# Kernel optimization log

Hardware: AMD Instinct MI355X
Metric: run time of the kernel (lower is better)

Reference implementation:

```python
import jax, jax.numpy as jnp
import numpy as np

N = 96
M = 96
# visual field constants
L_V_EX, S_V_EX, L_V_IN, S_V_IN = 1.6, 3.5, 1.23, 6.3
FV, TAU_V, UPS_V, P_V, K_V = 1.0, 3.0, 3.0, 0.3, 7.0
# auditory field constants
L_A_EX, S_A_EX, L_A_IN, S_A_IN = 1.0, 5.3, 0.8, 11.8
FA, TAU_A, UPS_A, P_A, K_A = 1.0, 3.0, 3.0, 0.3, 3.0
# multisensory field constants
L_M_EX, S_M_EX, L_M_IN, S_M_IN = 3.8, 3.5, 3.3, 6.2
TAU_M, UPS_M, P_M = 3.0, 3.0, 0.3


def _torus_sqdist():
    # squared toroidal distance components: dx2[i,h], dy2[j,k]
    ii = jnp.arange(N, dtype=jnp.float32)
    jj = jnp.arange(M, dtype=jnp.float32)
    dx = jnp.abs(ii[:, None] - ii[None, :])
    dx = jnp.minimum(dx, N - dx)
    dy = jnp.abs(jj[:, None] - jj[None, :])
    dy = jnp.minimum(dy, M - dy)
    # aux[i,j,h,k] = dx[i,h]^2 + dy[j,k]^2
    return dx[:, None, :, None] ** 2 + dy[None, :, None, :] ** 2


def _dog(aux, l_ex, s_ex, l_in, s_in):
    # Faithful to source: exp(-aux/2 * sigma**2) == exp(-0.5*aux*sigma^2)
    return l_ex * jnp.exp(-0.5 * aux * (s_ex ** 2)) - l_in * jnp.exp(-0.5 * aux * (s_in ** 2))


def setup_inputs() -> dict:
    key = jax.random.key(0)
    ks = jax.random.split(key, 7)
    return {
        "video": jax.random.normal(ks[0], (32, 1024), dtype=jnp.float32),
        "audio": jax.random.normal(ks[1], (32, 2048), dtype=jnp.float32),
        "rf_v": jax.random.normal(ks[2], (N, M, 1024), dtype=jnp.float32) * (1.0 / np.sqrt(1024.0)),
        "rf_a": jax.random.normal(ks[3], (N, M, 2048), dtype=jnp.float32) * (1.0 / np.sqrt(2048.0)),
        "na_v": jax.random.normal(ks[4], (N, M), dtype=jnp.float32),
        "na_a": jax.random.normal(ks[5], (N, M), dtype=jnp.float32),
        "na_m": jax.random.normal(ks[6], (N, M), dtype=jnp.float32),
    }


def reference(video, audio, rf_v, rf_a, na_v, na_a, na_m):
    aux = _torus_sqdist()  # (N, M, N, M)
    syn_v = _dog(aux, L_V_EX, S_V_EX, L_V_IN, S_V_IN)
    syn_a = _dog(aux, L_A_EX, S_A_EX, L_A_IN, S_A_IN)
    syn_m = _dog(aux, L_M_EX, S_M_EX, L_M_IN, S_M_IN)

    # external inputs: sum over feature dim -> (B, N, M)
    ext_v = jnp.einsum('bv,ijv->bij', video, rf_v)
    ext_a = jnp.einsum('ba,ija->bij', audio, rf_a)

    # all-pairs neighbor inputs: neighbor[i,j] = sum_{h,k} act[h,k] * syn[i,j,h,k]
    nb_v = jnp.einsum('ijhk,hk->ij', syn_v, na_v)
    nb_a = jnp.einsum('ijhk,hk->ij', syn_a, na_a)

    coll_v = FV * na_m
    coll_a = FA * na_m

    na_v_new = na_v * (TAU_V - 1.0) / TAU_V + (1.0 / TAU_V) * jax.nn.sigmoid(
        (ext_v + nb_v - UPS_V + coll_v) * P_V)  # (B, N, M)
    na_a_new = na_a * (TAU_A - 1.0) / TAU_A + (1.0 / TAU_A) * jax.nn.sigmoid(
        (ext_a + nb_a - UPS_A + coll_a) * P_A)  # (B, N, M)

    nb_m = jnp.einsum('ijhk,hk->ij', syn_m, na_m)
    na_m_new = na_m * (TAU_M - 1.0) / TAU_M + (1.0 / TAU_M) * jax.nn.sigmoid(
        (K_V * na_v_new + K_A * na_a_new + nb_m - UPS_M) * P_M)  # (B, N, M)
    return na_m_new
```

## Files before the change

kernel.cpp:

```cpp
#include <hip/hip_runtime.h>
#include <math.h>

#define NN   96
#define NPOS (96*96)
#define BB   32
#define KV   1024
#define KA   2048

#define EXTV_OFF  0
#define EXTA0_OFF (BB*NPOS)
#define EXTA1_OFF (2*BB*NPOS)
#define CPT_OFF   (3*BB*NPOS)
#define AFV_OFF   (CPT_OFF + 6*NPOS)
#define AFV_SLOTS ((KV/32)*2*64)
#define AFA_OFF   (AFV_OFF + AFV_SLOTS*4)
#define AFA_SLOTS ((KA/32)*2*64)

typedef __bf16 bf16x8 __attribute__((ext_vector_type(8)));
typedef __bf16 bf16x4 __attribute__((ext_vector_type(4)));
typedef float  f32x4  __attribute__((ext_vector_type(4)));

__global__ __launch_bounds__(256) void nbT_kernel(
    const float* __restrict__ na_v, const float* __restrict__ na_a,
    const float* __restrict__ na_m, const float* __restrict__ video,
    const float* __restrict__ audio, float* __restrict__ ws)
{
    __shared__ float G[96][100];
    __shared__ float act_s[96][100];
    __shared__ float T1t[24][100];

    if (blockIdx.x >= 24) {
        const int e = (blockIdx.x - 24) * 256 + threadIdx.x;
        const float* src; bf16x8* dst; int K, el;
        if (e < AFV_SLOTS) { src = video; K = KV; dst = (bf16x8*)(ws + AFV_OFF); el = e; }
        else               { src = audio; K = KA; dst = (bf16x8*)(ws + AFA_OFF); el = e - AFV_SLOTS; }
        const int l  = el & 63;
        const int hb = (el >> 6) & 1;
        const int sg = el >> 7;
        const int b  = hb * 16 + (l & 15);
        const int k0 = sg * 32 + ((l >> 4) << 3);
        const float4 f0 = *(const float4*)&src[(size_t)b * K + k0];
        const float4 f1 = *(const float4*)&src[(size_t)b * K + k0 + 4];
        bf16x8 v;
        v[0] = (__bf16)f0.x; v[1] = (__bf16)f0.y; v[2] = (__bf16)f0.z; v[3] = (__bf16)f0.w;
        v[4] = (__bf16)f1.x; v[5] = (__bf16)f1.y; v[6] = (__bf16)f1.z; v[7] = (__bf16)f1.w;
        dst[el] = v;
        return;
    }

    const int c  = blockIdx.x >> 2;
    const int js = (blockIdx.x & 3) * 24;
    float l, s;
    if      (c == 0) { l =  1.60f; s = 3.5f;  }
    else if (c == 1) { l = -1.23f; s = 6.3f;  }
    else if (c == 2) { l =  1.00f; s = 5.3f;  }
    else if (c == 3) { l = -0.80f; s = 11.8f; }
    else if (c == 4) { l =  3.80f; s = 3.5f;  }
    else             { l = -3.30f; s = 6.2f;  }
    const float s2 = s * s;
    const int f = c >> 1;
    const float* act = (f == 0) ? na_v : (f == 1) ? na_a : na_m;
    const int tid = threadIdx.x;
    float* cpt = ws + CPT_OFF;

    for (int idx = tid; idx < 9216; idx += 256) {
        int j = idx / 96, k = idx - j * 96;
        int d = abs(j - k); d = min(d, 96 - d);
        G[j][k]     = __expf(-0.5f * (float)(d * d) * s2);
        act_s[j][k] = act[idx];
    }
    __syncthreads();

    const int hg3 = (tid >> 3) * 3;
    const int jl3 = (tid & 7) * 3;

    float t1[3][3] = {};
    for (int k0 = 0; k0 < 96; k0 += 4) {
        float4 av[3], gv[3];
        #pragma unroll
        for (int r = 0; r < 3; r++) {
            av[r] = *(const float4*)&act_s[hg3 + r][k0];
            gv[r] = *(const float4*)&G[js + jl3 + r][k0];
        }
        #pragma unroll
        for (int hh = 0; hh < 3; hh++)
            #pragma unroll
            for (int jj = 0; jj < 3; jj++)
                t1[hh][jj] += av[hh].x * gv[jj].x + av[hh].y * gv[jj].y
                            + av[hh].z * gv[jj].z + av[hh].w * gv[jj].w;
    }
    #pragma unroll
    for (int hh = 0; hh < 3; hh++)
        #pragma unroll
        for (int jj = 0; jj < 3; jj++)
            T1t[jl3 + jj][hg3 + hh] = t1[hh][jj];
    __syncthreads();

    float o[3][3] = {};
    for (int h0 = 0; h0 < 96; h0 += 4) {
        float4 gv[3], tv[3];
        #pragma unroll
        for (int r = 0; r < 3; r++) {
            gv[r] = *(const float4*)&G[hg3 + r][h0];
            tv[r] = *(const float4*)&T1t[jl3 + r][h0];
        }
        #pragma unroll
        for (int ii = 0; ii < 3; ii++)
            #pragma unroll
            for (int jj = 0; jj < 3; jj++)
                o[ii][jj] += gv[ii].x * tv[jj].x + gv[ii].y * tv[jj].y
                           + gv[ii].z * tv[jj].z + gv[ii].w * tv[jj].w;
    }
    #pragma unroll
    for (int ii = 0; ii < 3; ii++)
        #pragma unroll
        for (int jj = 0; jj < 3; jj++)
            cpt[c * NPOS + (hg3 + ii) * 96 + (js + jl3 + jj)] = l * o[ii][jj];
}

#define LDS_ROW 2064
#define RED_OFF (16*LDS_ROW)
__global__ __launch_bounds__(512, 4) void ext_mfma(
    const float* __restrict__ rf_v, const float* __restrict__ rf_a,
    float* __restrict__ ws)
{
    __shared__ char lds[16 * LDS_ROW + 6144];
    const int tid = threadIdx.x;
    const int bid = blockIdx.x;

    const float* rf; const bf16x8* af; float* ext; int K, kb, pt;
    if (bid < 1152) {
        const int c = bid / 576; pt = bid - c * 576;
        rf = rf_a; K = KA; kb = c << 10;
        af  = (const bf16x8*)(ws + AFA_OFF);
        ext = ws + EXTA0_OFF + c * (BB * NPOS);
    } else {
        pt = bid - 1152; rf = rf_v; K = KV; kb = 0;
        af  = (const bf16x8*)(ws + AFV_OFF);
        ext = ws + EXTV_OFF;
    }

    {
        const int r0 = tid >> 8;
        const int c4 = (tid & 255) * 4;
        float4 fa[8];
        #pragma unroll
        for (int u = 0; u < 8; ++u)
            fa[u] = *(const float4*)(rf + (size_t)(pt * 16 + r0 + 2 * u) * K + kb + c4);
        #pragma unroll
        for (int u = 0; u < 8; ++u) {
            bf16x4 v;
            v[0] = (__bf16)fa[u].x; v[1] = (__bf16)fa[u].y;
            v[2] = (__bf16)fa[u].z; v[3] = (__bf16)fa[u].w;
            *(bf16x4*)(lds + (r0 + 2 * u) * LDS_ROW + c4 * 2) = v;
        }
    }
    __syncthreads();

    const int l  = tid & 63, w = tid >> 6;
    const int bh = w & 1, kq = w >> 1;
    const bf16x8* ap = af + ((kb >> 5) + kq * 8) * 128 + (bh << 6) + l;
    const char*   bp = lds + (l & 15) * LDS_ROW + kq * 512 + ((l >> 4) << 4);

    bf16x8 a0 = ap[0 * 128], a1 = ap[1 * 128], a2 = ap[2 * 128], a3 = ap[3 * 128];
    bf16x8 a4 = ap[4 * 128], a5 = ap[5 * 128], a6 = ap[6 * 128], a7 = ap[7 * 128];
    bf16x8 b0 = *(const bf16x8*)(bp + 0 * 64), b1 = *(const bf16x8*)(bp + 1 * 64);
    bf16x8 b2 = *(const bf16x8*)(bp + 2 * 64), b3 = *(const bf16x8*)(bp + 3 * 64);
    bf16x8 b4 = *(const bf16x8*)(bp + 4 * 64), b5 = *(const bf16x8*)(bp + 5 * 64);
    bf16x8 b6 = *(const bf16x8*)(bp + 6 * 64), b7 = *(const bf16x8*)(bp + 7 * 64);

    f32x4 acc = {0.f, 0.f, 0.f, 0.f};
    acc = __builtin_amdgcn_mfma_f32_16x16x32_bf16(a0, b0, acc, 0, 0, 0);
    acc = __builtin_amdgcn_mfma_f32_16x16x32_bf16(a1, b1, acc, 0, 0, 0);
    acc = __builtin_amdgcn_mfma_f32_16x16x32_bf16(a2, b2, acc, 0, 0, 0);
    acc = __builtin_amdgcn_mfma_f32_16x16x32_bf16(a3, b3, acc, 0, 0, 0);
    acc = __builtin_amdgcn_mfma_f32_16x16x32_bf16(a4, b4, acc, 0, 0, 0);
    acc = __builtin_amdgcn_mfma_f32_16x16x32_bf16(a5, b5, acc, 0, 0, 0);
    acc = __builtin_amdgcn_mfma_f32_16x16x32_bf16(a6, b6, acc, 0, 0, 0);
    acc = __builtin_amdgcn_mfma_f32_16x16x32_bf16(a7, b7, acc, 0, 0, 0);

    if (kq) *(f32x4*)(lds + RED_OFF + (((kq - 1) << 1) + bh) * 1024 + l * 16) = acc;
    __syncthreads();
    if (!kq) {
        #pragma unroll
        for (int q = 0; q < 3; ++q)
            acc += *(const f32x4*)(lds + RED_OFF + ((q << 1) + bh) * 1024 + l * 16);
        const int pcol = pt * 16 + (l & 15);
        const int br0  = (bh << 4) + ((l >> 4) << 2);
        #pragma unroll
        for (int r = 0; r < 4; ++r)
            ext[(size_t)(br0 + r) * NPOS + pcol] = acc[r];
    }
}

__global__ __launch_bounds__(256) void combine_kernel(
    const float* __restrict__ na_v, const float* __restrict__ na_a,
    const float* __restrict__ na_m, const float* __restrict__ ws,
    float* __restrict__ out)
{
    const int npq = NPOS >> 2;
    const int t = blockIdx.x * 256 + threadIdx.x;
    if (t >= BB * npq) return;
    const int b  = t / npq;
    const int p0 = (t - b * npq) << 2;

    float4 ev  = *(const float4*)&ws[EXTV_OFF  + (size_t)b * NPOS + p0];
    float4 ea0 = *(const float4*)&ws[EXTA0_OFF + (size_t)b * NPOS + p0];
    float4 ea1 = *(const float4*)&ws[EXTA1_OFF + (size_t)b * NPOS + p0];
    float4 ea = {ea0.x + ea1.x, ea0.y + ea1.y, ea0.z + ea1.z, ea0.w + ea1.w};
    const float* cpt = ws + CPT_OFF;
    float4 q0 = *(const float4*)&cpt[0 * NPOS + p0];
    float4 q1 = *(const float4*)&cpt[1 * NPOS + p0];
    float4 q2 = *(const float4*)&cpt[2 * NPOS + p0];
    float4 q3 = *(const float4*)&cpt[3 * NPOS + p0];
    float4 q4 = *(const float4*)&cpt[4 * NPOS + p0];
    float4 q5 = *(const float4*)&cpt[5 * NPOS + p0];
    float4 nv = *(const float4*)&na_v[p0];
    float4 na = *(const float4*)&na_a[p0];
    float4 nm = *(const float4*)&na_m[p0];

    float evs[4] = {ev.x, ev.y, ev.z, ev.w};
    float eas[4] = {ea.x, ea.y, ea.z, ea.w};
    float nbv[4] = {q0.x + q1.x, q0.y + q1.y, q0.z + q1.z, q0.w + q1.w};
    float nba[4] = {q2.x + q3.x, q2.y + q3.y, q2.z + q3.z, q2.w + q3.w};
    float nbm[4] = {q4.x + q5.x, q4.y + q5.y, q4.z + q5.z, q4.w + q5.w};
    float nvs[4] = {nv.x, nv.y, nv.z, nv.w};
    float nas[4] = {na.x, na.y, na.z, na.w};
    float nms[4] = {nm.x, nm.y, nm.z, nm.w};

    float4 o;
    float* os = (float*)&o;
    #pragma unroll
    for (int u = 0; u < 4; u++) {
        const float xv = (evs[u] + nbv[u] - 3.0f + nms[u]) * 0.3f;
        const float nav_new = nvs[u] * (2.f / 3.f) + (1.f / 3.f) / (1.f + __expf(-xv));
        const float xa = (eas[u] + nba[u] - 3.0f + nms[u]) * 0.3f;
        const float naa_new = nas[u] * (2.f / 3.f) + (1.f / 3.f) / (1.f + __expf(-xa));
        const float xm = (7.0f * nav_new + 3.0f * naa_new + nbm[u] - 3.0f) * 0.3f;
        os[u] = nms[u] * (2.f / 3.f) + (1.f / 3.f) / (1.f + __expf(-xm));
    }
    *(float4*)&out[(size_t)b * NPOS + p0] = o;
}

extern "C" void kernel_launch(void* const* d_in, const int* in_sizes, int n_in,
                              void* d_out, int out_size, void* d_ws, size_t ws_size,
                              hipStream_t stream) {
    const float* video = (const float*)d_in[0];
    const float* audio = (const float*)d_in[1];
    const float* rf_v  = (const float*)d_in[2];
    const float* rf_a  = (const float*)d_in[3];
    const float* na_v  = (const float*)d_in[4];
    const float* na_a  = (const float*)d_in[5];
    const float* na_m  = (const float*)d_in[6];
    float* ws  = (float*)d_ws;
    float* out = (float*)d_out;

    nbT_kernel<<<72, 256, 0, stream>>>(na_v, na_a, na_m, video, audio, ws);
    ext_mfma<<<1728, 512, 0, stream>>>(rf_v, rf_a, ws);
    combine_kernel<<<(BB * NPOS / 4 + 255) / 256, 256, 0, stream>>>(
        na_v, na_a, na_m, ws, out);
}
```

Measured before the change: 38.08 us.

## Merge ext GEMM blocks per position tile with double-buffered LDS pipeline

The ext_mfma kernel now launches one block per 16-position tile, replacing the earlier three blocks per tile (two audio K halves plus video). Each block walks six K-chunks of 512 through a double-buffered LDS stage, overlapping the global loads of the next chunk with the MFMA work on the current one. Because the audio result is reduced within a single block, the separate EXTA1 partial buffer is no longer needed and combine_kernel reads one audio value instead of two. The cost is fewer blocks (576), so less parallelism to hide memory latency on a large GPU, plus more barriers per block.

Result: slower. 44.71 us (+17.4%).

```diff
diff --git a/kernel.cpp b/kernel.cpp
--- a/kernel.cpp
+++ b/kernel.cpp
@@ -8,7 +8,7 @@
 #define KA   2048
 
 #define EXTV_OFF  0
-#define EXTA0_OFF (BB*NPOS)
+#define EXTA_OFF  (BB*NPOS)
 #define EXTA1_OFF (2*BB*NPOS)
 #define CPT_OFF   (3*BB*NPOS)
 #define AFV_OFF   (CPT_OFF + 6*NPOS)
@@ -118,79 +118,130 @@
             cpt[c * NPOS + (hg3 + ii) * 96 + (js + jl3 + jj)] = l * o[ii][jj];
 }
 
-#define LDS_ROW 2064
-#define RED_OFF (16*LDS_ROW)
+#define LROW 1040
+#define BUFSZ (16*LROW)
+#define REDOFF (2*BUFSZ)
 __global__ __launch_bounds__(512, 4) void ext_mfma(
     const float* __restrict__ rf_v, const float* __restrict__ rf_a,
     float* __restrict__ ws)
 {
-    __shared__ char lds[16 * LDS_ROW + 6144];
+    __shared__ char lds[2 * BUFSZ + 6144];
     const int tid = threadIdx.x;
-    const int bid = blockIdx.x;
-
-    const float* rf; const bf16x8* af; float* ext; int K, kb, pt;
-    if (bid < 1152) {
-        const int c = bid / 576; pt = bid - c * 576;
-        rf = rf_a; K = KA; kb = c << 10;
-        af  = (const bf16x8*)(ws + AFA_OFF);
-        ext = ws + EXTA0_OFF + c * (BB * NPOS);
-    } else {
-        pt = bid - 1152; rf = rf_v; K = KV; kb = 0;
-        af  = (const bf16x8*)(ws + AFV_OFF);
-        ext = ws + EXTV_OFF;
-    }
-
-    {
-        const int r0 = tid >> 8;
-        const int c4 = (tid & 255) * 4;
-        float4 fa[8];
-        #pragma unroll
-        for (int u = 0; u < 8; ++u)
-            fa[u] = *(const float4*)(rf + (size_t)(pt * 16 + r0 + 2 * u) * K + kb + c4);
-        #pragma unroll
-        for (int u = 0; u < 8; ++u) {
-            bf16x4 v;
-            v[0] = (__bf16)fa[u].x; v[1] = (__bf16)fa[u].y;
-            v[2] = (__bf16)fa[u].z; v[3] = (__bf16)fa[u].w;
-            *(bf16x4*)(lds + (r0 + 2 * u) * LDS_ROW + c4 * 2) = v;
-        }
-    }
-    __syncthreads();
-
+    const int pt  = blockIdx.x;
+    const int p0  = pt * 16;
+
+    const int r    = tid >> 7;
+    const int c128 = tid & 127;
     const int l  = tid & 63, w = tid >> 6;
     const int bh = w & 1, kq = w >> 1;
-    const bf16x8* ap = af + ((kb >> 5) + kq * 8) * 128 + (bh << 6) + l;
-    const char*   bp = lds + (l & 15) * LDS_ROW + kq * 512 + ((l >> 4) << 4);
-
-    bf16x8 a0 = ap[0 * 128], a1 = ap[1 * 128], a2 = ap[2 * 128], a3 = ap[3 * 128];
-    bf16x8 a4 = ap[4 * 128], a5 = ap[5 * 128], a6 = ap[6 * 128], a7 = ap[7 * 128];
-    bf16x8 b0 = *(const bf16x8*)(bp + 0 * 64), b1 = *(const bf16x8*)(bp + 1 * 64);
-    bf16x8 b2 = *(const bf16x8*)(bp + 2 * 64), b3 = *(const bf16x8*)(bp + 3 * 64);
-    bf16x8 b4 = *(const bf16x8*)(bp + 4 * 64), b5 = *(const bf16x8*)(bp + 5 * 64);
-    bf16x8 b6 = *(const bf16x8*)(bp + 6 * 64), b7 = *(const bf16x8*)(bp + 7 * 64);
-
-    f32x4 acc = {0.f, 0.f, 0.f, 0.f};
-    acc = __builtin_amdgcn_mfma_f32_16x16x32_bf16(a0, b0, acc, 0, 0, 0);
-    acc = __builtin_amdgcn_mfma_f32_16x16x32_bf16(a1, b1, acc, 0, 0, 0);
-    acc = __builtin_amdgcn_mfma_f32_16x16x32_bf16(a2, b2, acc, 0, 0, 0);
-    acc = __builtin_amdgcn_mfma_f32_16x16x32_bf16(a3, b3, acc, 0, 0, 0);
-    acc = __builtin_amdgcn_mfma_f32_16x16x32_bf16(a4, b4, acc, 0, 0, 0);
-    acc = __builtin_amdgcn_mfma_f32_16x16x32_bf16(a5, b5, acc, 0, 0, 0);
-    acc = __builtin_amdgcn_mfma_f32_16x16x32_bf16(a6, b6, acc, 0, 0, 0);
-    acc = __builtin_amdgcn_mfma_f32_16x16x32_bf16(a7, b7, acc, 0, 0, 0);
-
-    if (kq) *(f32x4*)(lds + RED_OFF + (((kq - 1) << 1) + bh) * 1024 + l * 16) = acc;
-    __syncthreads();
-    if (!kq) {
-        #pragma unroll
-        for (int q = 0; q < 3; ++q)
-            acc += *(const f32x4*)(lds + RED_OFF + ((q << 1) + bh) * 1024 + l * 16);
-        const int pcol = pt * 16 + (l & 15);
-        const int br0  = (bh << 4) + ((l >> 4) << 2);
-        #pragma unroll
-        for (int r = 0; r < 4; ++r)
-            ext[(size_t)(br0 + r) * NPOS + pcol] = acc[r];
-    }
+    const int rb_off = (l & 15) * LROW + kq * 256 + ((l >> 4) << 4);
+
+    const float*  sb[6];
+    const bf16x8* ab[6];
+    {
+        const float* ra = rf_a + (size_t)(p0 + r) * KA + c128 * 4;
+        const float* rv = rf_v + (size_t)(p0 + r) * KV + c128 * 4;
+        sb[0] = ra;        sb[1] = ra + 512;
+        sb[2] = ra + 1024; sb[3] = ra + 1536;
+        sb[4] = rv;        sb[5] = rv + 512;
+        const bf16x8* aa = (const bf16x8*)(ws + AFA_OFF) + kq * 4 * 128 + (bh << 6) + l;
+        const bf16x8* av = (const bf16x8*)(ws + AFV_OFF) + kq * 4 * 128 + (bh << 6) + l;
+        ab[0] = aa;        ab[1] = aa + 16 * 128;
+        ab[2] = aa + 32 * 128; ab[3] = aa + 48 * 128;
+        ab[4] = av;        ab[5] = av + 16 * 128;
+    }
+
+    float4 fa0, fa1, fa2, fa3;
+    bf16x8 xA0, xA1, xA2, xA3, xB0, xB1, xB2, xB3;
+    f32x4 accA = {0.f, 0.f, 0.f, 0.f};
+    f32x4 accV = {0.f, 0.f, 0.f, 0.f};
+
+#define STAGE(S, KK) do {                                         \
+        fa0 = *(const float4*)(sb[S]);                            \
+        fa1 = *(const float4*)(sb[S] + 4  * (size_t)(KK));        \
+        fa2 = *(const float4*)(sb[S] + 8  * (size_t)(KK));        \
+        fa3 = *(const float4*)(sb[S] + 12 * (size_t)(KK));        \
+    } while (0)
+
+#define CVT4(F) ({ bf16x4 v_;                                     \
+        v_[0] = (__bf16)(F).x; v_[1] = (__bf16)(F).y;             \
+        v_[2] = (__bf16)(F).z; v_[3] = (__bf16)(F).w; v_; })
+
+#define WWRITE(S) do {                                            \
+        char* bw = lds + ((S) & 1) * BUFSZ + c128 * 8;            \
+        *(bf16x4*)(bw + (r +  0) * LROW) = CVT4(fa0);             \
+        *(bf16x4*)(bw + (r +  4) * LROW) = CVT4(fa1);             \
+        *(bf16x4*)(bw + (r +  8) * LROW) = CVT4(fa2);             \
+        *(bf16x4*)(bw + (r + 12) * LROW) = CVT4(fa3);             \
+    } while (0)
+
+#define AFLD(S, A0, A1, A2, A3) do {                              \
+        const bf16x8* ap_ = ab[S];                                \
+        A0 = ap_[0]; A1 = ap_[128]; A2 = ap_[256]; A3 = ap_[384]; \
+    } while (0)
+
+#define COMP(S, ACC, A0, A1, A2, A3) do {                                      \
+        const char* br = lds + ((S) & 1) * BUFSZ + rb_off;                     \
+        bf16x8 b0 = *(const bf16x8*)(br);                                      \
+        bf16x8 b1 = *(const bf16x8*)(br + 64);                                 \
+        bf16x8 b2 = *(const bf16x8*)(br + 128);                                \
+        bf16x8 b3 = *(const bf16x8*)(br + 192);                                \
+        ACC = __builtin_amdgcn_mfma_f32_16x16x32_bf16(A0, b0, ACC, 0, 0, 0);   \
+        ACC = __builtin_amdgcn_mfma_f32_16x16x32_bf16(A1, b1, ACC, 0, 0, 0);   \
+        ACC = __builtin_amdgcn_mfma_f32_16x16x32_bf16(A2, b2, ACC, 0, 0, 0);   \
+        ACC = __builtin_amdgcn_mfma_f32_16x16x32_bf16(A3, b3, ACC, 0, 0, 0);   \
+    } while (0)
+
+#define BARL do {                                                 \
+        asm volatile("s_waitcnt lgkmcnt(0)" ::: "memory");        \
+        __builtin_amdgcn_sched_barrier(0);                        \
+        __builtin_amdgcn_s_barrier();                             \
+        __builtin_amdgcn_sched_barrier(0);                        \
+    } while (0)
+
+#define REDUCE(ACC, EXTP) do {                                                 \
+        if (kq) *(f32x4*)(lds + REDOFF + (((kq - 1) << 1) + bh) * 1024         \
+                          + l * 16) = ACC;                                     \
+        BARL;                                                                  \
+        if (!kq) {                                                             \
+            ACC += *(const f32x4*)(lds + REDOFF + (0 * 2 + bh) * 1024 + l*16); \
+            ACC += *(const f32x4*)(lds + REDOFF + (1 * 2 + bh) * 1024 + l*16); \
+            ACC += *(const f32x4*)(lds + REDOFF + (2 * 2 + bh) * 1024 + l*16); \
+            const int pcol = p0 + (l & 15);                                    \
+            const int br0  = (bh << 4) + ((l >> 4) << 2);                      \
+            float* ep = (EXTP);                                                \
+            ep[(size_t)(br0 + 0) * NPOS + pcol] = ACC[0];                      \
+            ep[(size_t)(br0 + 1) * NPOS + pcol] = ACC[1];                      \
+            ep[(size_t)(br0 + 2) * NPOS + pcol] = ACC[2];                      \
+            ep[(size_t)(br0 + 3) * NPOS + pcol] = ACC[3];                      \
+        }                                                                      \
+    } while (0)
+
+    STAGE(0, KA); AFLD(0, xA0, xA1, xA2, xA3);
+    WWRITE(0);
+    STAGE(1, KA);
+    BARL;
+    COMP(0, accA, xA0, xA1, xA2, xA3); AFLD(1, xB0, xB1, xB2, xB3);
+    WWRITE(1); STAGE(2, KA); BARL;
+    COMP(1, accA, xB0, xB1, xB2, xB3); AFLD(2, xA0, xA1, xA2, xA3);
+    WWRITE(2); STAGE(3, KA); BARL;
+    COMP(2, accA, xA0, xA1, xA2, xA3); AFLD(3, xB0, xB1, xB2, xB3);
+    WWRITE(3); STAGE(4, KV); BARL;
+    COMP(3, accA, xB0, xB1, xB2, xB3); AFLD(4, xA0, xA1, xA2, xA3);
+    REDUCE(accA, ws + EXTA_OFF);
+    WWRITE(4); STAGE(5, KV); BARL;
+    COMP(4, accV, xA0, xA1, xA2, xA3); AFLD(5, xB0, xB1, xB2, xB3);
+    WWRITE(5); BARL;
+    COMP(5, accV, xB0, xB1, xB2, xB3);
+    REDUCE(accV, ws + EXTV_OFF);
+
+#undef STAGE
+#undef CVT4
+#undef WWRITE
+#undef AFLD
+#undef COMP
+#undef BARL
+#undef REDUCE
 }
 
 __global__ __launch_bounds__(256) void combine_kernel(
@@ -204,10 +255,8 @@
     const int b  = t / npq;
     const int p0 = (t - b * npq) << 2;
 
-    float4 ev  = *(const float4*)&ws[EXTV_OFF  + (size_t)b * NPOS + p0];
-    float4 ea0 = *(const float4*)&ws[EXTA0_OFF + (size_t)b * NPOS + p0];
-    float4 ea1 = *(const float4*)&ws[EXTA1_OFF + (size_t)b * NPOS + p0];
-    float4 ea = {ea0.x + ea1.x, ea0.y + ea1.y, ea0.z + ea1.z, ea0.w + ea1.w};
+    float4 ev = *(const float4*)&ws[EXTV_OFF + (size_t)b * NPOS + p0];
+    float4 ea = *(const float4*)&ws[EXTA_OFF + (size_t)b * NPOS + p0];
     const float* cpt = ws + CPT_OFF;
     float4 q0 = *(const float4*)&cpt[0 * NPOS + p0];
     float4 q1 = *(const float4*)&cpt[1 * NPOS + p0];
@@ -256,7 +305,7 @@
     float* out = (float*)d_out;
 
     nbT_kernel<<<72, 256, 0, stream>>>(na_v, na_a, na_m, video, audio, ws);
-    ext_mfma<<<1728, 512, 0, stream>>>(rf_v, rf_a, ws);
+    ext_mfma<<<576, 512, 0, stream>>>(rf_v, rf_a, ws);
     combine_kernel<<<(BB * NPOS / 4 + 255) / 256, 256, 0, stream>>>(
         na_v, na_a, na_m, ws, out);
 }
```
